# Performance work log

Hardware: AMD Instinct MI355X
Metric: run time of the kernel (lower is better)

Reference implementation:

```python
import jax, jax.numpy as jnp
import numpy as np

D_MODEL = 1024
NUM_HEADS = 16
HEAD_DIM = D_MODEL // NUM_HEADS
THETA = 10000.0


def setup_inputs() -> dict:
    key = jax.random.key(0)
    k1, k2, k3 = jax.random.split(key, 3)
    B, S = 4, 2048
    std_qkv = (2.0 / (D_MODEL + 3 * D_MODEL)) ** 0.5
    std_out = (2.0 / (D_MODEL + D_MODEL)) ** 0.5
    return {
        "x": jax.random.normal(k1, (B, S, D_MODEL), dtype=jnp.float32),
        "token_positions": jnp.arange(S, dtype=jnp.int64 if jax.config.jax_enable_x64 else jnp.int32),
        "w_qkv": jax.random.normal(k2, (3 * D_MODEL, D_MODEL), dtype=jnp.float32) * std_qkv,
        "w_out": jax.random.normal(k3, (D_MODEL, D_MODEL), dtype=jnp.float32) * std_out,
    }


def _apply_rope(x, token_positions):
    # x: [b, h, s, d_h]; token_positions: [s]
    inv_freq = 1.0 / (THETA ** (jnp.arange(0, HEAD_DIM, 2, dtype=jnp.float32) / HEAD_DIM))
    angles = token_positions.astype(jnp.float32)[:, None] * inv_freq  # [s, d_h/2]
    cos, sin = jnp.cos(angles), jnp.sin(angles)
    x_even = x[..., 0::2]
    x_odd = x[..., 1::2]
    out_even = x_even * cos - x_odd * sin
    out_odd = x_even * sin + x_odd * cos
    # re-interleave even/odd lanes
    return jnp.stack([out_even, out_odd], axis=-1).reshape(x.shape)


def reference(x, token_positions, w_qkv, w_out):
    B, S, _ = x.shape
    qkv = jnp.einsum("bsd,ed->bse", x, w_qkv)  # [b, s, 3*d_model]
    q, k, v = jnp.split(qkv, 3, axis=-1)

    def to_heads(t):  # [b, s, d_model] -> [b, h, s, d_h]
        return t.reshape(B, S, NUM_HEADS, HEAD_DIM).transpose(0, 2, 1, 3)

    q, k, v = to_heads(q), to_heads(k), to_heads(v)
    q = _apply_rope(q, token_positions)
    k = _apply_rope(k, token_positions)

    scale = 1.0 / (HEAD_DIM ** 0.5)
    scores = jnp.einsum("bhqd,bhkd->bhqk", q, k) * scale  # [b, h, s, s]
    causal = jnp.tril(jnp.ones((S, S), dtype=bool))
    scores = jnp.where(causal, scores, -jnp.inf)
    probs = jax.nn.softmax(scores, axis=-1)
    out = jnp.einsum("bhqk,bhkd->bhqd", probs, v)  # [b, h, s, d_h]
    out = out.transpose(0, 2, 1, 3).reshape(B, S, D_MODEL)
    return jnp.einsum("bsd,ed->bse", out, w_out)
```

## Files before the change

kernel.cpp:

```cpp
#include <hip/hip_runtime.h>

typedef unsigned short u16;
typedef __attribute__((ext_vector_type(4))) float f32x4;
typedef __attribute__((ext_vector_type(8))) __bf16 bf16x8;
typedef __attribute__((ext_vector_type(8))) short short8;
typedef __attribute__((ext_vector_type(4))) u16 u16x4;

__device__ __forceinline__ u16 f2bf(float f) {
    union { float f; unsigned u; } v; v.f = f;
    unsigned r = v.u + 0x7fffu + ((v.u >> 16) & 1u);
    return (u16)(r >> 16);
}

__device__ __forceinline__ f32x4 mfma16(bf16x8 a, bf16x8 b, f32x4 c) {
    return __builtin_amdgcn_mfma_f32_16x16x32_bf16(a, b, c, 0, 0, 0);
}

__device__ __forceinline__ void gload16(const u16* g, u16* lds) {
    __builtin_amdgcn_global_load_lds(
        (const __attribute__((address_space(1))) void*)g,
        (__attribute__((address_space(3))) void*)lds, 16, 0, 0);
}

__global__ void cvt_bf16_kernel(const float* __restrict__ src, u16* __restrict__ dst, int n4) {
    int i = blockIdx.x * blockDim.x + threadIdx.x;
    if (i >= n4) return;
    float4 v = ((const float4*)src)[i];
    u16x4 o = { f2bf(v.x), f2bf(v.y), f2bf(v.z), f2bf(v.w) };
    *(u16x4*)&dst[i * 4] = o;
}

__global__ void rope_tbl_kernel(const int* __restrict__ pos, float2* __restrict__ tbl) {
    int i = blockIdx.x * blockDim.x + threadIdx.x;
    int s = i >> 5, p = i & 31;
    float inv = powf(10000.0f, -(float)p / 32.0f);
    float a = (float)pos[s] * inv;
    float sn, cs;
    sincosf(a, &sn, &cs);
    tbl[i] = make_float2(cs, sn);
}

template<int MODE>
__global__ __launch_bounds__(256) void gemm_bt(
    const u16* __restrict__ A, const u16* __restrict__ B,
    float* __restrict__ C, int N,
    u16* __restrict__ Qt, u16* __restrict__ Ktn, u16* __restrict__ VTt,
    const float2* __restrict__ tbl)
{
    __shared__ alignas(16) u16 As[128 * 32];
    __shared__ alignas(16) u16 Bs[128 * 32];
    const int t = threadIdx.x;
    const int l = t & 63, w = t >> 6;
    const int lg = l >> 4, lc = l & 15;
    const int wr = w >> 1, wc = w & 1;
    const int brow = blockIdx.y * 128, bcol = blockIdx.x * 128;
    const int sr = w * 16 + (l >> 2), sc = (l & 3) * 8;
    const u16* ga = A + (size_t)(brow + sr) * 1024 + sc;
    const u16* gb = B + (size_t)(bcol + sr) * 1024 + sc;
    u16* la = &As[w * 512];
    u16* lb = &Bs[w * 512];
    f32x4 acc[4][4] = {};

    for (int kt = 0; kt < 1024; kt += 32) {
        __syncthreads();
        gload16(ga + kt, la);
        gload16(ga + 64 * 1024 + kt, la + 2048);
        gload16(gb + kt, lb);
        gload16(gb + 64 * 1024 + kt, lb + 2048);
        __syncthreads();
        bf16x8 af[4], bfr[4];
#pragma unroll
        for (int i = 0; i < 4; ++i)
            af[i] = *(const bf16x8*)&As[(wr * 64 + i * 16 + lc) * 32 + lg * 8];
#pragma unroll
        for (int j = 0; j < 4; ++j)
            bfr[j] = *(const bf16x8*)&Bs[(wc * 64 + j * 16 + lc) * 32 + lg * 8];
#pragma unroll
        for (int i = 0; i < 4; ++i)
#pragma unroll
            for (int j = 0; j < 4; ++j)
                acc[i][j] = mfma16(af[i], bfr[j], acc[i][j]);
    }

    if (MODE == 0) {
#pragma unroll
        for (int i = 0; i < 4; ++i) {
            int row = brow + wr * 64 + i * 16 + lg * 4;
#pragma unroll
            for (int j = 0; j < 4; ++j) {
                int col = bcol + wc * 64 + j * 16 + lc;
#pragma unroll
                for (int jj = 0; jj < 4; ++jj)
                    C[(size_t)(row + jj) * N + col] = acc[i][j][jj];
            }
        }
    } else {
        const int b = brow >> 11;
#pragma unroll
        for (int i = 0; i < 4; ++i) {
            int s0 = (brow & 2047) + wr * 64 + i * 16 + lg * 4;
#pragma unroll
            for (int j = 0; j < 4; ++j) {
                int e0 = bcol + wc * 64 + j * 16;
                int region = e0 >> 10;
                int er = e0 & 1023;
                int h = er >> 6;
                int d = (er & 63) + lc;
                size_t bh = (size_t)(b * 16 + h);
                if (region <= 1) {
                    int p = d >> 1;
                    float sgn = (d & 1) ? 1.0f : -1.0f;
                    u16* dst = (region == 0) ? Qt : Ktn;
                    float mul = (region == 0) ? 0.18033688011112043f : 1.0f;
#pragma unroll
                    for (int jj = 0; jj < 4; ++jj) {
                        float v = acc[i][j][jj];
                        float pr = __shfl_xor(v, 1);
                        float2 cs = tbl[(size_t)(s0 + jj) * 32 + p];
                        float o = (v * cs.x + pr * cs.y * sgn) * mul;
                        int s = s0 + jj;
                        int dd = (region == 0) ? d : (d ^ ((s & 7) << 3));
                        dst[((size_t)bh * 2048 + s) * 64 + dd] = f2bf(o);
                    }
                } else {
                    int tile = s0 >> 6, r = s0 & 63;
                    int p0 = ((r >> 5) << 5) + (((r >> 2) & 3) << 3) + (((r >> 4) & 1) << 2);
                    int idx = (tile << 6) + (p0 ^ ((d & 7) << 3));
                    u16x4 pk;
#pragma unroll
                    for (int jj = 0; jj < 4; ++jj) pk[jj] = f2bf(acc[i][j][jj]);
                    *(u16x4*)&VTt[((size_t)bh * 64 + d) * 2048 + idx] = pk;
                }
            }
        }
    }
}

__global__ __launch_bounds__(128, 4) void attn_kernel(
    const u16* __restrict__ Qt, const u16* __restrict__ Kswz,
    const u16* __restrict__ Vp, u16* __restrict__ O)
{
    __shared__ alignas(16) u16 Kl[64 * 64];
    __shared__ alignas(16) u16 Vl[64 * 64];
    const int bid = blockIdx.x;
    const int qt = 31 - (bid >> 6);
    const int bh = bid & 63;
    const int t = threadIdx.x, l = t & 63, w = t >> 6;
    const int lg = l >> 4, lc = l & 15;
    const int qb0 = qt * 64 + w * 32;
    const int ntiles = qt + 1;
    const int swz = (lc & 7) << 3;

    bf16x8 qf[2][2];
#pragma unroll
    for (int f = 0; f < 2; ++f)
#pragma unroll
        for (int fk = 0; fk < 2; ++fk)
            qf[f][fk] = *(const bf16x8*)&Qt[((size_t)bh * 2048 + qb0 + 16 * f + lc) * 64 + fk * 32 + lg * 8];

    const bf16x8 ones = { (__bf16)1.f, (__bf16)1.f, (__bf16)1.f, (__bf16)1.f,
                          (__bf16)1.f, (__bf16)1.f, (__bf16)1.f, (__bf16)1.f };

    f32x4 aco[2][4] = {};
    f32x4 aco_sum[2] = {};
    float m[2] = { -1e30f, -1e30f };

    const int sr = l >> 3;
    const int scq = (l & 7) * 8;
    const u16* gK = Kswz + (size_t)bh * 131072 + scq;
    const u16* gV = Vp + (size_t)bh * 131072 + scq;

    for (int kt = 0; kt < ntiles; ++kt) {
        const int kv0 = kt * 64;
        __syncthreads();
#pragma unroll
        for (int j = 0; j < 4; ++j) {
            const int rb = w * 32 + j * 8;
            gload16(gK + (((size_t)(kv0 + rb + sr)) << 6), &Kl[rb * 64]);
            gload16(gV + (size_t)(rb + sr) * 2048 + kv0, &Vl[rb * 64]);
        }
        __syncthreads();

        f32x4 sc[2][4];
        const f32x4 zf = { 0.f, 0.f, 0.f, 0.f };
#pragma unroll
        for (int nb = 0; nb < 4; ++nb) {
            const u16* kr = &Kl[(nb * 16 + lc) * 64];
            bf16x8 kb0 = *(const bf16x8*)&kr[(lg * 8) ^ swz];
            bf16x8 kb1 = *(const bf16x8*)&kr[(32 + lg * 8) ^ swz];
            sc[0][nb] = mfma16(kb0, qf[0][0], zf);
            sc[0][nb] = mfma16(kb1, qf[0][1], sc[0][nb]);
            sc[1][nb] = mfma16(kb0, qf[1][0], zf);
            sc[1][nb] = mfma16(kb1, qf[1][1], sc[1][nb]);
        }

        float pm[2];
#pragma unroll
        for (int f = 0; f < 2; ++f) {
            if (kv0 + 63 > qb0 + 16 * f) {
                const int qq = qb0 + 16 * f + lc;
#pragma unroll
                for (int nb = 0; nb < 4; ++nb) {
                    const int kb = kv0 + nb * 16 + lg * 4;
#pragma unroll
                    for (int jj = 0; jj < 4; ++jj)
                        if (kb + jj > qq) sc[f][nb][jj] = -1e38f;
                }
            }
            float a0 = fmaxf(fmaxf(sc[f][0][0], sc[f][0][1]), fmaxf(sc[f][0][2], sc[f][0][3]));
            float a1 = fmaxf(fmaxf(sc[f][1][0], sc[f][1][1]), fmaxf(sc[f][1][2], sc[f][1][3]));
            float a2 = fmaxf(fmaxf(sc[f][2][0], sc[f][2][1]), fmaxf(sc[f][2][2], sc[f][2][3]));
            float a3 = fmaxf(fmaxf(sc[f][3][0], sc[f][3][1]), fmaxf(sc[f][3][2], sc[f][3][3]));
            float a = fmaxf(fmaxf(a0, a1), fmaxf(a2, a3));
            a = fmaxf(a, __shfl_xor(a, 16));
            a = fmaxf(a, __shfl_xor(a, 32));
            pm[f] = a;
        }

        int need = (pm[0] > m[0] + 11.0f) || (pm[1] > m[1] + 11.0f);
        if (__any(need)) {
#pragma unroll
            for (int f = 0; f < 2; ++f) {
                float mn = fmaxf(m[f], pm[f]);
                float scal = exp2f(m[f] - mn);
                m[f] = mn;
                aco_sum[f][0] *= scal;
#pragma unroll
                for (int nb = 0; nb < 4; ++nb) aco[f][nb] *= scal;
            }
        }

        bf16x8 pB[2][2];
#pragma unroll
        for (int f = 0; f < 2; ++f) {
#pragma unroll
            for (int nb = 0; nb < 4; ++nb)
#pragma unroll
                for (int jj = 0; jj < 4; ++jj)
                    sc[f][nb][jj] = exp2f(sc[f][nb][jj] - m[f]);
#pragma unroll
            for (int fk = 0; fk < 2; ++fk) {
                bf16x8 pb;
#pragma unroll
                for (int e = 0; e < 4; ++e) {
                    pb[e]     = (__bf16)sc[f][2 * fk][e];
                    pb[e + 4] = (__bf16)sc[f][2 * fk + 1][e];
                }
                pB[f][fk] = pb;
            }
        }

#pragma unroll
        for (int nb = 0; nb < 4; ++nb) {
            const u16* vr = &Vl[(nb * 16 + lc) * 64];
#pragma unroll
            for (int fk = 0; fk < 2; ++fk) {
                bf16x8 va = *(const bf16x8*)&vr[(fk * 32 + lg * 8) ^ swz];
                aco[0][nb] = mfma16(va, pB[0][fk], aco[0][nb]);
                aco[1][nb] = mfma16(va, pB[1][fk], aco[1][nb]);
            }
        }
#pragma unroll
        for (int f = 0; f < 2; ++f) {
            aco_sum[f] = mfma16(ones, pB[f][0], aco_sum[f]);
            aco_sum[f] = mfma16(ones, pB[f][1], aco_sum[f]);
        }
    }

    const int b = bh >> 4, h = bh & 15;
#pragma unroll
    for (int f = 0; f < 2; ++f) {
        float rinv = 1.0f / aco_sum[f][0];
        size_t row = (size_t)b * 2048 + qb0 + 16 * f + lc;
#pragma unroll
        for (int nb = 0; nb < 4; ++nb) {
            u16x4 pk;
#pragma unroll
            for (int jj = 0; jj < 4; ++jj) pk[jj] = f2bf(aco[f][nb][jj] * rinv);
            *(u16x4*)&O[row * 1024 + h * 64 + nb * 16 + lg * 4] = pk;
        }
    }
}

extern "C" void kernel_launch(void* const* d_in, const int* in_sizes, int n_in,
                              void* d_out, int out_size, void* d_ws, size_t ws_size,
                              hipStream_t stream) {
    const float* x    = (const float*)d_in[0];
    const int*   pos  = (const int*)d_in[1];
    const float* wqkv = (const float*)d_in[2];
    const float* wout = (const float*)d_in[3];
    float* out = (float*)d_out;
    char* ws = (char*)d_ws;

    u16*    x_bf    = (u16*)(ws);
    u16*    wqkv_bf = (u16*)(ws + 16777216);
    u16*    wout_bf = (u16*)(ws + 23068672);
    float2* tbl     = (float2*)(ws + 25165824);
    u16*    Qt      = (u16*)(ws + 25690112);
    u16*    Kt      = (u16*)(ws + 42467328);
    u16*    VTt     = (u16*)(ws + 59244544);
    u16*    O       = (u16*)(ws + 76021760);
    if (ws_size < 92798976u) return;

    cvt_bf16_kernel<<<8192, 256, 0, stream>>>(x, x_bf, 2097152);
    cvt_bf16_kernel<<<3072, 256, 0, stream>>>(wqkv, wqkv_bf, 786432);
    cvt_bf16_kernel<<<1024, 256, 0, stream>>>(wout, wout_bf, 262144);
    rope_tbl_kernel<<<256, 256, 0, stream>>>(pos, tbl);

    dim3 g1(24, 64);
    gemm_bt<1><<<g1, 256, 0, stream>>>(x_bf, wqkv_bf, nullptr, 0, Qt, Kt, VTt, tbl);

    attn_kernel<<<2048, 128, 0, stream>>>(Qt, Kt, VTt, O);

    dim3 g2(8, 64);
    gemm_bt<0><<<g2, 256, 0, stream>>>(O, wout_bf, out, 1024, nullptr, nullptr, nullptr, nullptr);
}
```

Before: 320.6 us.

## Double-buffer K/V tiles and widen attention blocks to 128 query rows

The attention kernel now uses 256 threads (4 waves) per block covering 128 query rows, which halves the grid and shares each staged K/V tile across twice as many queries. K/V tiles are double-buffered in LDS: the next tile's global-to-LDS load is issued before computing on the current one, leaving one barrier per iteration instead of two. Waves whose query rows lie entirely before a tile skip its compute but still join the barriers. In exchange, LDS use doubles, and the lower-indexed waves in each block sit idle on the last causal tiles, which adds imbalance.

```diff
diff --git a/kernel.cpp b/kernel.cpp
--- a/kernel.cpp
+++ b/kernel.cpp
@@ -136,19 +136,19 @@
     }
 }
 
-__global__ __launch_bounds__(128, 4) void attn_kernel(
+__global__ __launch_bounds__(256, 4) void attn_kernel(
     const u16* __restrict__ Qt, const u16* __restrict__ Kswz,
     const u16* __restrict__ Vp, u16* __restrict__ O)
 {
-    __shared__ alignas(16) u16 Kl[64 * 64];
-    __shared__ alignas(16) u16 Vl[64 * 64];
+    __shared__ alignas(16) u16 Kl[2][64 * 64];
+    __shared__ alignas(16) u16 Vl[2][64 * 64];
     const int bid = blockIdx.x;
-    const int qt = 31 - (bid >> 6);
+    const int qt = 15 - (bid >> 6);
     const int bh = bid & 63;
     const int t = threadIdx.x, l = t & 63, w = t >> 6;
     const int lg = l >> 4, lc = l & 15;
-    const int qb0 = qt * 64 + w * 32;
-    const int ntiles = qt + 1;
+    const int qb0 = qt * 128 + w * 32;
+    const int ntiles = 2 * qt + 2;
     const int swz = (lc & 7) << 3;
 
     bf16x8 qf[2][2];
@@ -165,106 +165,118 @@
     f32x4 aco_sum[2] = {};
     float m[2] = { -1e30f, -1e30f };
 
-    const int sr = l >> 3;
-    const int scq = (l & 7) * 8;
-    const u16* gK = Kswz + (size_t)bh * 131072 + scq;
-    const u16* gV = Vp + (size_t)bh * 131072 + scq;
+    const int srow = t >> 3;
+    const int scol = (t & 7) * 8;
+    const u16* gK = Kswz + (size_t)bh * 131072;
+    const u16* gV = Vp + (size_t)bh * 131072;
+
+    auto stage = [&](int buf, int kv0) {
+        gload16(gK + ((size_t)(kv0 + srow) << 6) + scol,      &Kl[buf][srow * 64 + scol]);
+        gload16(gK + ((size_t)(kv0 + srow + 32) << 6) + scol, &Kl[buf][(srow + 32) * 64 + scol]);
+        gload16(gV + (size_t)srow * 2048 + kv0 + scol,        &Vl[buf][srow * 64 + scol]);
+        gload16(gV + (size_t)(srow + 32) * 2048 + kv0 + scol, &Vl[buf][(srow + 32) * 64 + scol]);
+    };
+
+    stage(0, 0);
+    __syncthreads();
+    int cur = 0;
 
     for (int kt = 0; kt < ntiles; ++kt) {
         const int kv0 = kt * 64;
+        if (kt + 1 < ntiles) stage(cur ^ 1, kv0 + 64);
+
+        if (kv0 <= qb0 + 31) {
+            const u16* Kc = Kl[cur];
+            const u16* Vc = Vl[cur];
+
+            f32x4 sc[2][4];
+            const f32x4 zf = { 0.f, 0.f, 0.f, 0.f };
+#pragma unroll
+            for (int nb = 0; nb < 4; ++nb) {
+                const u16* kr = &Kc[(nb * 16 + lc) * 64];
+                bf16x8 kb0 = *(const bf16x8*)&kr[(lg * 8) ^ swz];
+                bf16x8 kb1 = *(const bf16x8*)&kr[(32 + lg * 8) ^ swz];
+                sc[0][nb] = mfma16(kb0, qf[0][0], zf);
+                sc[0][nb] = mfma16(kb1, qf[0][1], sc[0][nb]);
+                sc[1][nb] = mfma16(kb0, qf[1][0], zf);
+                sc[1][nb] = mfma16(kb1, qf[1][1], sc[1][nb]);
+            }
+
+            float pm[2];
+#pragma unroll
+            for (int f = 0; f < 2; ++f) {
+                if (kv0 + 63 > qb0 + 16 * f) {
+                    const int qq = qb0 + 16 * f + lc;
+#pragma unroll
+                    for (int nb = 0; nb < 4; ++nb) {
+                        const int kb = kv0 + nb * 16 + lg * 4;
+#pragma unroll
+                        for (int jj = 0; jj < 4; ++jj)
+                            if (kb + jj > qq) sc[f][nb][jj] = -1e38f;
+                    }
+                }
+                float a0 = fmaxf(fmaxf(sc[f][0][0], sc[f][0][1]), fmaxf(sc[f][0][2], sc[f][0][3]));
+                float a1 = fmaxf(fmaxf(sc[f][1][0], sc[f][1][1]), fmaxf(sc[f][1][2], sc[f][1][3]));
+                float a2 = fmaxf(fmaxf(sc[f][2][0], sc[f][2][1]), fmaxf(sc[f][2][2], sc[f][2][3]));
+                float a3 = fmaxf(fmaxf(sc[f][3][0], sc[f][3][1]), fmaxf(sc[f][3][2], sc[f][3][3]));
+                float a = fmaxf(fmaxf(a0, a1), fmaxf(a2, a3));
+                a = fmaxf(a, __shfl_xor(a, 16));
+                a = fmaxf(a, __shfl_xor(a, 32));
+                pm[f] = a;
+            }
+
+            int need = (pm[0] > m[0] + 11.0f) || (pm[1] > m[1] + 11.0f);
+            if (__any(need)) {
+#pragma unroll
+                for (int f = 0; f < 2; ++f) {
+                    float mn = fmaxf(m[f], pm[f]);
+                    float scal = exp2f(m[f] - mn);
+                    m[f] = mn;
+                    aco_sum[f][0] *= scal;
+#pragma unroll
+                    for (int nb = 0; nb < 4; ++nb) aco[f][nb] *= scal;
+                }
+            }
+
+            bf16x8 pB[2][2];
+#pragma unroll
+            for (int f = 0; f < 2; ++f) {
+#pragma unroll
+                for (int nb = 0; nb < 4; ++nb)
+#pragma unroll
+                    for (int jj = 0; jj < 4; ++jj)
+                        sc[f][nb][jj] = exp2f(sc[f][nb][jj] - m[f]);
+#pragma unroll
+                for (int fk = 0; fk < 2; ++fk) {
+                    bf16x8 pb;
+#pragma unroll
+                    for (int e = 0; e < 4; ++e) {
+                        pb[e]     = (__bf16)sc[f][2 * fk][e];
+                        pb[e + 4] = (__bf16)sc[f][2 * fk + 1][e];
+                    }
+                    pB[f][fk] = pb;
+                }
+            }
+
+#pragma unroll
+            for (int nb = 0; nb < 4; ++nb) {
+                const u16* vr = &Vc[(nb * 16 + lc) * 64];
+#pragma unroll
+                for (int fk = 0; fk < 2; ++fk) {
+                    bf16x8 va = *(const bf16x8*)&vr[(fk * 32 + lg * 8) ^ swz];
+                    aco[0][nb] = mfma16(va, pB[0][fk], aco[0][nb]);
+                    aco[1][nb] = mfma16(va, pB[1][fk], aco[1][nb]);
+                }
+            }
+#pragma unroll
+            for (int f = 0; f < 2; ++f) {
+                aco_sum[f] = mfma16(ones, pB[f][0], aco_sum[f]);
+                aco_sum[f] = mfma16(ones, pB[f][1], aco_sum[f]);
+            }
+        }
+
         __syncthreads();
-#pragma unroll
-        for (int j = 0; j < 4; ++j) {
-            const int rb = w * 32 + j * 8;
-            gload16(gK + (((size_t)(kv0 + rb + sr)) << 6), &Kl[rb * 64]);
-            gload16(gV + (size_t)(rb + sr) * 2048 + kv0, &Vl[rb * 64]);
-        }
-        __syncthreads();
-
-        f32x4 sc[2][4];
-        const f32x4 zf = { 0.f, 0.f, 0.f, 0.f };
-#pragma unroll
-        for (int nb = 0; nb < 4; ++nb) {
-            const u16* kr = &Kl[(nb * 16 + lc) * 64];
-            bf16x8 kb0 = *(const bf16x8*)&kr[(lg * 8) ^ swz];
-            bf16x8 kb1 = *(const bf16x8*)&kr[(32 + lg * 8) ^ swz];
-            sc[0][nb] = mfma16(kb0, qf[0][0], zf);
-            sc[0][nb] = mfma16(kb1, qf[0][1], sc[0][nb]);
-            sc[1][nb] = mfma16(kb0, qf[1][0], zf);
-            sc[1][nb] = mfma16(kb1, qf[1][1], sc[1][nb]);
-        }
-
-        float pm[2];
-#pragma unroll
-        for (int f = 0; f < 2; ++f) {
-            if (kv0 + 63 > qb0 + 16 * f) {
-                const int qq = qb0 + 16 * f + lc;
-#pragma unroll
-                for (int nb = 0; nb < 4; ++nb) {
-                    const int kb = kv0 + nb * 16 + lg * 4;
-#pragma unroll
-                    for (int jj = 0; jj < 4; ++jj)
-                        if (kb + jj > qq) sc[f][nb][jj] = -1e38f;
-                }
-            }
-            float a0 = fmaxf(fmaxf(sc[f][0][0], sc[f][0][1]), fmaxf(sc[f][0][2], sc[f][0][3]));
-            float a1 = fmaxf(fmaxf(sc[f][1][0], sc[f][1][1]), fmaxf(sc[f][1][2], sc[f][1][3]));
-            float a2 = fmaxf(fmaxf(sc[f][2][0], sc[f][2][1]), fmaxf(sc[f][2][2], sc[f][2][3]));
-            float a3 = fmaxf(fmaxf(sc[f][3][0], sc[f][3][1]), fmaxf(sc[f][3][2], sc[f][3][3]));
-            float a = fmaxf(fmaxf(a0, a1), fmaxf(a2, a3));
-            a = fmaxf(a, __shfl_xor(a, 16));
-            a = fmaxf(a, __shfl_xor(a, 32));
-            pm[f] = a;
-        }
-
-        int need = (pm[0] > m[0] + 11.0f) || (pm[1] > m[1] + 11.0f);
-        if (__any(need)) {
-#pragma unroll
-            for (int f = 0; f < 2; ++f) {
-                float mn = fmaxf(m[f], pm[f]);
-                float scal = exp2f(m[f] - mn);
-                m[f] = mn;
-                aco_sum[f][0] *= scal;
-#pragma unroll
-                for (int nb = 0; nb < 4; ++nb) aco[f][nb] *= scal;
-            }
-        }
-
-        bf16x8 pB[2][2];
-#pragma unroll
-        for (int f = 0; f < 2; ++f) {
-#pragma unroll
-            for (int nb = 0; nb < 4; ++nb)
-#pragma unroll
-                for (int jj = 0; jj < 4; ++jj)
-                    sc[f][nb][jj] = exp2f(sc[f][nb][jj] - m[f]);
-#pragma unroll
-            for (int fk = 0; fk < 2; ++fk) {
-                bf16x8 pb;
-#pragma unroll
-                for (int e = 0; e < 4; ++e) {
-                    pb[e]     = (__bf16)sc[f][2 * fk][e];
-                    pb[e + 4] = (__bf16)sc[f][2 * fk + 1][e];
-                }
-                pB[f][fk] = pb;
-            }
-        }
-
-#pragma unroll
-        for (int nb = 0; nb < 4; ++nb) {
-            const u16* vr = &Vl[(nb * 16 + lc) * 64];
-#pragma unroll
-            for (int fk = 0; fk < 2; ++fk) {
-                bf16x8 va = *(const bf16x8*)&vr[(fk * 32 + lg * 8) ^ swz];
-                aco[0][nb] = mfma16(va, pB[0][fk], aco[0][nb]);
-                aco[1][nb] = mfma16(va, pB[1][fk], aco[1][nb]);
-            }
-        }
-#pragma unroll
-        for (int f = 0; f < 2; ++f) {
-            aco_sum[f] = mfma16(ones, pB[f][0], aco_sum[f]);
-            aco_sum[f] = mfma16(ones, pB[f][1], aco_sum[f]);
-        }
+        cur ^= 1;
     }
 
     const int b = bh >> 4, h = bh & 15;
@@ -310,7 +322,7 @@
     dim3 g1(24, 64);
     gemm_bt<1><<<g1, 256, 0, stream>>>(x_bf, wqkv_bf, nullptr, 0, Qt, Kt, VTt, tbl);
 
-    attn_kernel<<<2048, 128, 0, stream>>>(Qt, Kt, VTt, O);
+    attn_kernel<<<1024, 256, 0, stream>>>(Qt, Kt, VTt, O);
 
     dim3 g2(8, 64);
     gemm_bt<0><<<g2, 256, 0, stream>>>(O, wout_bf, out, 1024, nullptr, nullptr, nullptr, nullptr);
```

Result: faster. 310.0 us (-3.3%).
